# Kernel tuning notes

Hardware: AMD Instinct MI355X
Metric: run time of the kernel (lower is better)

The kernel has to match this reference:

```python
import jax, jax.numpy as jnp
import numpy as np

B, C, D, H, W = 1, 192, 32, 32, 32
NUM_HEADS = 6
KSZ = 3
DILATIONS = (1, 2, 3)
ND = len(DILATIONS)
HPD = NUM_HEADS // ND          # heads per dilation
HEAD_DIM = C // NUM_HEADS      # 32
CPD = C // ND                  # channels per dilation = HPD * HEAD_DIM
SCALE = HEAD_DIM ** -0.5
HIDDEN = int(C * 4.0)


def setup_inputs() -> dict:
    key = jax.random.key(0)
    ks = jax.random.split(key, 12)
    s = 0.02
    return {
        "x": jax.random.normal(ks[0], (B, C, H, W, D), jnp.float32),
        "qkv_w": jax.random.normal(ks[1], (3 * C, C), jnp.float32) * s,
        "proj_w": jax.random.normal(ks[2], (C, C), jnp.float32) * s,
        "proj_b": jnp.zeros((C,), jnp.float32),
        "g1": jnp.ones((C,), jnp.float32),
        "be1": jnp.zeros((C,), jnp.float32),
        "g2": jnp.ones((C,), jnp.float32),
        "be2": jnp.zeros((C,), jnp.float32),
        "w1": jax.random.normal(ks[3], (C, HIDDEN), jnp.float32) * s,
        "b1": jnp.zeros((HIDDEN,), jnp.float32),
        "w2": jax.random.normal(ks[4], (HIDDEN, C), jnp.float32) * s,
        "b2": jnp.zeros((C,), jnp.float32),
    }


def _layernorm(x, g, b, eps=1e-5):
    mu = jnp.mean(x, -1, keepdims=True)
    var = jnp.mean(jnp.square(x - mu), -1, keepdims=True)
    return (x - mu) * jax.lax.rsqrt(var + eps) * g + b


def _unfold3d(x, k, r):
    # x: [B, c, D, H, W] -> [k^3, B, c, D, H, W] of dilated local neighborhoods
    p = r * (k - 1) // 2
    xp = jnp.pad(x, ((0, 0), (0, 0), (p, p), (p, p), (p, p)))
    d, h, w = x.shape[2:]
    sl = [xp[:, :, i:i + d, j:j + h, l:l + w]
          for i in range(0, k * r, r)
          for j in range(0, k * r, r)
          for l in range(0, k * r, r)]
    return jnp.stack(sl, 0)


def _attn(x, qkv_w, proj_w, proj_b):
    # x: [B, D, H, W, C]
    x_cf = jnp.transpose(x, (0, 4, 1, 2, 3))                   # [B,C,D,H,W]
    qkv = jnp.einsum('oc,bczyx->bozyx', qkv_w, x_cf)
    qkv = qkv.reshape(B, 3, ND, CPD, D, H, W)
    outs = []
    for i, r in enumerate(DILATIONS):
        q = qkv[:, 0, i].reshape(B, HPD, HEAD_DIM, D, H, W)
        ku = _unfold3d(qkv[:, 1, i], KSZ, r).reshape(KSZ ** 3, B, HPD, HEAD_DIM, D, H, W)
        vu = _unfold3d(qkv[:, 2, i], KSZ, r).reshape(KSZ ** 3, B, HPD, HEAD_DIM, D, H, W)
        a = jnp.einsum('bnezyx,kbnezyx->bnzyxk', q, ku) * SCALE  # [B,n,D,H,W,27]
        a = jax.nn.softmax(a, axis=-1)
        o = jnp.einsum('bnzyxk,kbnezyx->bzyxne', a, vu).reshape(B, D, H, W, CPD)
        outs.append(o)
    out = jnp.concatenate(outs, -1)                            # [B,D,H,W,C] dilation-major
    return out @ proj_w + proj_b


def reference(x, qkv_w, proj_w, proj_b, g1, be1, g2, be2, w1, b1, w2, b2):
    # x: [B, C, H, W, D] -> [B, D, H, W, C]
    h = jnp.transpose(x, (0, 4, 2, 3, 1))
    h = h + _attn(_layernorm(h, g1, be1), qkv_w, proj_w, proj_b)
    m = _layernorm(h, g2, be2)
    m = jax.nn.gelu(m @ w1 + b1, approximate=False) @ w2 + b2
    h = h + m
    return jnp.transpose(h, (0, 4, 2, 3, 1))
```

## Files before the change

### kernel.cpp

```cpp
#include <hip/hip_runtime.h>
#include <hip/hip_bf16.h>
#include <math.h>

#define NV     32768
#define HIDDEN 768
#define SCALE  0.17677669529663687f

typedef __attribute__((ext_vector_type(8))) short short8;
typedef __attribute__((ext_vector_type(4))) float floatx4;
typedef __hip_bfloat16 bf16;

__device__ __forceinline__ void gload16(const void* g, void* l) {
    __builtin_amdgcn_global_load_lds(
        (const __attribute__((address_space(1))) unsigned int*)g,
        (__attribute__((address_space(3))) unsigned int*)l, 16, 0, 0);
}

__device__ __forceinline__ float bf2f(short s) {
    unsigned u = ((unsigned)(unsigned short)s) << 16;
    return __builtin_bit_cast(float, u);
}
__device__ __forceinline__ short f2bfs(float f) {
    bf16 b = __float2bfloat16(f);
    return *reinterpret_cast<short*>(&b);
}

__global__ __launch_bounds__(256) void prep_kernel(
        const float* __restrict__ qkv_w, const float* __restrict__ proj_w,
        const float* __restrict__ w1, const float* __restrict__ w2,
        bf16* __restrict__ wqkv, bf16* __restrict__ wproj,
        bf16* __restrict__ w1t, bf16* __restrict__ w2t) {
    int i = blockIdx.x * 256 + threadIdx.x;
    if (i < 110592) {
        wqkv[i] = (bf16)qkv_w[i];
    } else if (i < 147456) {
        int j = i - 110592; int r = j / 192, c = j - r * 192;
        wproj[c * 192 + r] = (bf16)proj_w[j];
    } else if (i < 294912) {
        int j = i - 147456; int r = j / 768, c = j - r * 768;
        w1t[c * 192 + r] = (bf16)w1[j];
    } else if (i < 442368) {
        int j = i - 294912; int r = j / 192, c = j - r * 192;
        w2t[c * 768 + r] = (bf16)w2[j];
    }
}

__global__ __launch_bounds__(256) void tin_ln_kernel(
        const float* __restrict__ xin, const float* __restrict__ g,
        const float* __restrict__ be, bf16* __restrict__ h,
        bf16* __restrict__ lnb) {
    __shared__ float lds[32 * 193];
    int yx = blockIdx.x;
    int y = yx >> 5, x = yx & 31;
    for (int idx = threadIdx.x; idx < 192 * 32; idx += 256) {
        int c = idx >> 5, z = idx & 31;
        lds[z * 193 + c] = xin[(((size_t)c * 32 + y) * 32 + x) * 32 + z];
    }
    __syncthreads();
    int wave = threadIdx.x >> 6, lane = threadIdx.x & 63;
    float ga = g[lane], gb = g[lane + 64], gc = g[lane + 128];
    float ba = be[lane], bb = be[lane + 64], bc = be[lane + 128];
    for (int z = wave; z < 32; z += 4) {
        float x0 = lds[z * 193 + lane];
        float x1 = lds[z * 193 + lane + 64];
        float x2 = lds[z * 193 + lane + 128];
        float s = x0 + x1 + x2;
        #pragma unroll
        for (int m = 32; m; m >>= 1) s += __shfl_xor(s, m);
        float mu = s * (1.f / 192.f);
        float d0 = x0 - mu, d1 = x1 - mu, d2 = x2 - mu;
        float s2 = d0 * d0 + d1 * d1 + d2 * d2;
        #pragma unroll
        for (int m = 32; m; m >>= 1) s2 += __shfl_xor(s2, m);
        float rstd = rsqrtf(s2 * (1.f / 192.f) + 1e-5f);
        size_t v = (size_t)((z << 10) + (y << 5) + x) * 192;
        h[v + lane]         = (bf16)x0;
        h[v + lane + 64]    = (bf16)x1;
        h[v + lane + 128]   = (bf16)x2;
        lnb[v + lane]       = (bf16)(d0 * rstd * ga + ba);
        lnb[v + lane + 64]  = (bf16)(d1 * rstd * gb + bb);
        lnb[v + lane + 128] = (bf16)(d2 * rstd * gc + bc);
    }
}

__global__ __launch_bounds__(256) void tout_kernel(const bf16* __restrict__ h,
                                                   float* __restrict__ outp) {
    __shared__ float lds[32 * 193];
    int yx = blockIdx.x;
    int y = yx >> 5, x = yx & 31;
    for (int idx = threadIdx.x; idx < 32 * 192; idx += 256) {
        int z = idx / 192, c = idx - z * 192;
        lds[z * 193 + c] = __bfloat162float(h[((size_t)((z * 32 + y) * 32 + x)) * 192 + c]);
    }
    __syncthreads();
    for (int idx = threadIdx.x; idx < 192 * 32; idx += 256) {
        int c = idx >> 5, z = idx & 31;
        outp[(((size_t)c * 32 + y) * 32 + x) * 32 + z] = lds[z * 193 + c];
    }
}

template <int MODE>
__global__ __launch_bounds__(256, 2) void mgemm_kernel(
        const bf16* __restrict__ A,
        const bf16* __restrict__ Bw,
        void* __restrict__ Cp,
        const float* __restrict__ bias,
        const bf16* __restrict__ res,
        int M, int N, int K) {
    __shared__ short Asm[128 * 64];
    __shared__ short Bsm[64 * 64];
    const int tid = threadIdx.x;
    const int lane = tid & 63;
    const int wave = tid >> 6;
    const int wm = wave >> 1, wn = wave & 1;
    const int m0 = blockIdx.x * 128;
    const int n0 = blockIdx.y * 64;

    const int srow = lane >> 3;
    const int scol = ((lane & 7) ^ ((lane >> 3) & 7)) * 16;

    floatx4 acc[4][2] = {};

    for (int k0 = 0; k0 < K; k0 += 64) {
        #pragma unroll
        for (int s = 0; s < 4; ++s) {
            int seg = wave * 4 + s;
            const char* g = (const char*)(A + (size_t)(m0 + seg * 8 + srow) * K + k0) + scol;
            gload16(g, (char*)Asm + seg * 1024);
        }
        #pragma unroll
        for (int s = 0; s < 2; ++s) {
            int seg = wave * 2 + s;
            const char* g = (const char*)(Bw + (size_t)(n0 + seg * 8 + srow) * K + k0) + scol;
            gload16(g, (char*)Bsm + seg * 1024);
        }
        __syncthreads();
        #pragma unroll
        for (int ks = 0; ks < 2; ++ks) {
            short8 af[4], bfr[2];
            const int cb = ks * 64 + (lane >> 4) * 16;
            #pragma unroll
            for (int i = 0; i < 4; ++i) {
                int row = wm * 64 + i * 16 + (lane & 15);
                af[i] = *reinterpret_cast<const short8*>(
                    (const char*)Asm + row * 128 + (cb ^ ((row & 7) << 4)));
            }
            #pragma unroll
            for (int j = 0; j < 2; ++j) {
                int row = wn * 32 + j * 16 + (lane & 15);
                bfr[j] = *reinterpret_cast<const short8*>(
                    (const char*)Bsm + row * 128 + (cb ^ ((row & 7) << 4)));
            }
            #pragma unroll
            for (int i = 0; i < 4; ++i)
                #pragma unroll
                for (int j = 0; j < 2; ++j)
                    acc[i][j] = __builtin_amdgcn_mfma_f32_16x16x32_bf16(
                        af[i], bfr[j], acc[i][j], 0, 0, 0);
        }
        __syncthreads();
    }

    const int r4 = (lane >> 4) * 4;
    const int cc = lane & 15;
    #pragma unroll
    for (int i = 0; i < 4; ++i) {
        #pragma unroll
        for (int j = 0; j < 2; ++j) {
            int colg = n0 + wn * 32 + j * 16 + cc;
            float bv = (MODE == 1 || MODE == 2) ? bias[colg] : 0.f;
            #pragma unroll
            for (int rg = 0; rg < 4; ++rg) {
                int rowg = m0 + wm * 64 + i * 16 + r4 + rg;
                float v = acc[i][j][rg];
                if (MODE == 1 || MODE == 2) v += bv;
                if (MODE == 2) v = 0.5f * v * (1.f + erff(v * 0.70710678118654752f));
                if (MODE == 1) {
                    v += __bfloat162float(res[(size_t)rowg * N + colg]);
                    ((bf16*)Cp)[(size_t)rowg * N + colg] = (bf16)v;
                } else if (MODE == 2) {
                    ((bf16*)Cp)[(size_t)rowg * N + colg] = (bf16)v;
                } else {
                    int part = colg / 192;
                    int rem  = colg - part * 192;
                    int di   = rem >> 6, hc = rem & 63;
                    size_t addr = (size_t)part * (6 * (size_t)NV * 32)
                                + (size_t)((di << 1) + (hc >> 5)) * ((size_t)NV * 32)
                                + (size_t)rowg * 32 + (hc & 31);
                    ((bf16*)Cp)[addr] = (bf16)v;
                }
            }
        }
    }
}

__global__ __launch_bounds__(256) void projln_kernel(
        const bf16* __restrict__ A, const bf16* __restrict__ Bw,
        bf16* __restrict__ hres, bf16* __restrict__ lnout,
        const float* __restrict__ bias,
        const float* __restrict__ g2, const float* __restrict__ be2) {
    __shared__ short Asm[64 * 64];
    __shared__ short Bsm[192 * 64];
    const int tid = threadIdx.x;
    const int lane = tid & 63;
    const int wave = tid >> 6;
    const int m0 = blockIdx.x * 64;

    const int srow = lane >> 3;
    const int scol = ((lane & 7) ^ ((lane >> 3) & 7)) * 16;

    floatx4 acc[12] = {};

    for (int k0 = 0; k0 < 192; k0 += 64) {
        #pragma unroll
        for (int s = 0; s < 2; ++s) {
            int seg = wave * 2 + s;
            const char* g = (const char*)(A + (size_t)(m0 + seg * 8 + srow) * 192 + k0) + scol;
            gload16(g, (char*)Asm + seg * 1024);
        }
        #pragma unroll
        for (int s = 0; s < 6; ++s) {
            int seg = wave * 6 + s;
            const char* g = (const char*)(Bw + (size_t)(seg * 8 + srow) * 192 + k0) + scol;
            gload16(g, (char*)Bsm + seg * 1024);
        }
        __syncthreads();
        #pragma unroll
        for (int ks = 0; ks < 2; ++ks) {
            const int cb = ks * 64 + (lane >> 4) * 16;
            int arow = wave * 16 + (lane & 15);
            short8 af = *reinterpret_cast<const short8*>(
                (const char*)Asm + arow * 128 + (cb ^ ((arow & 7) << 4)));
            #pragma unroll
            for (int j = 0; j < 12; ++j) {
                int brow = j * 16 + (lane & 15);
                short8 bfr = *reinterpret_cast<const short8*>(
                    (const char*)Bsm + brow * 128 + (cb ^ ((brow & 7) << 4)));
                acc[j] = __builtin_amdgcn_mfma_f32_16x16x32_bf16(af, bfr, acc[j], 0, 0, 0);
            }
        }
        __syncthreads();
    }

    const int cc = lane & 15;
    #pragma unroll
    for (int rg = 0; rg < 4; ++rg) {
        int rowg = m0 + wave * 16 + (lane >> 4) * 4 + rg;
        float vals[12];
        float vsum = 0.f;
        #pragma unroll
        for (int j = 0; j < 12; ++j) {
            int col = j * 16 + cc;
            float v = acc[j][rg] + bias[col]
                    + __bfloat162float(hres[(size_t)rowg * 192 + col]);
            vals[j] = v;
            vsum += v;
        }
        #pragma unroll
        for (int m = 8; m; m >>= 1) vsum += __shfl_xor(vsum, m);
        float mu = vsum * (1.f / 192.f);
        float vsq = 0.f;
        #pragma unroll
        for (int j = 0; j < 12; ++j) {
            float d = vals[j] - mu;
            vsq += d * d;
        }
        #pragma unroll
        for (int m = 8; m; m >>= 1) vsq += __shfl_xor(vsq, m);
        float rstd = rsqrtf(vsq * (1.f / 192.f) + 1e-5f);
        #pragma unroll
        for (int j = 0; j < 12; ++j) {
            int col = j * 16 + cc;
            hres[(size_t)rowg * 192 + col] = (bf16)vals[j];
            lnout[(size_t)rowg * 192 + col] =
                (bf16)((vals[j] - mu) * rstd * g2[col] + be2[col]);
        }
    }
}

__global__ __launch_bounds__(256) void attn_kernel(
        const bf16* __restrict__ qa,
        const bf16* __restrict__ ka,
        const bf16* __restrict__ va,
        bf16* __restrict__ attn_out) {
    const int lin = blockIdx.x;
    const int swz = (lin & 7) * 384 + (lin >> 3);
    const int dh  = swz >> 9;
    const int rp  = swz & 511;
    const int di = dh >> 1;
    const int r  = di + 1;
    const int wave = threadIdx.x >> 6, lane = threadIdx.x & 63;
    const int yz = rp * 2 + (wave >> 1);
    const int z = yz >> 5, y = yz & 31;
    const int x = ((wave & 1) << 4) + (lane >> 2);
    const int co = (lane & 3) << 3;
    const int v = (z << 10) + (y << 5) + x;

    const bf16* qb = qa + (size_t)dh * NV * 32 + co;
    const bf16* kb = ka + (size_t)dh * NV * 32 + co;
    const bf16* vb = va + (size_t)dh * NV * 32 + co;

    float qf[8];
    {
        short8 qv = *reinterpret_cast<const short8*>(qb + (size_t)v * 32);
        #pragma unroll
        for (int u = 0; u < 8; ++u) qf[u] = bf2f(qv[u]);
    }

    float o[8];
    #pragma unroll
    for (int c = 0; c < 8; ++c) o[c] = 0.f;
    float denom = 0.f;
    const float cexp = SCALE * 1.44269504088896f;

    #pragma unroll
    for (int kk = 0; kk < 27; ++kk) {
        const int dz = kk / 9 - 1, dy = (kk / 3) % 3 - 1, dx = kk % 3 - 1;
        int nz = z + dz * r, ny = y + dy * r, nx = x + dx * r;
        bool ok = ((unsigned)nz < 32u) & ((unsigned)ny < 32u) & ((unsigned)nx < 32u);
        int nv = ok ? v + r * ((dz << 10) + (dy << 5) + dx) : v;
        short8 kv = *reinterpret_cast<const short8*>(kb + (size_t)nv * 32);
        short8 vv = *reinterpret_cast<const short8*>(vb + (size_t)nv * 32);
        float d = 0.f;
        #pragma unroll
        for (int u = 0; u < 8; ++u) d += qf[u] * bf2f(kv[u]);
        d += __shfl_xor(d, 1);
        d += __shfl_xor(d, 2);
        float p = exp2f(ok ? d * cexp : 0.f);
        denom += p;
        float w = ok ? p : 0.f;
        #pragma unroll
        for (int u = 0; u < 8; ++u) o[u] += w * bf2f(vv[u]);
    }
    float inv = 1.f / denom;

    bf16* op = attn_out + (size_t)v * 192 + di * 64 + (dh & 1) * 32 + co;
    short8 st;
    #pragma unroll
    for (int u = 0; u < 8; ++u) st[u] = f2bfs(o[u] * inv);
    *reinterpret_cast<short8*>(op) = st;
}

extern "C" void kernel_launch(void* const* d_in, const int* in_sizes, int n_in,
                              void* d_out, int out_size, void* d_ws, size_t ws_size,
                              hipStream_t stream) {
    const float* x      = (const float*)d_in[0];
    const float* qkv_w  = (const float*)d_in[1];
    const float* proj_w = (const float*)d_in[2];
    const float* proj_b = (const float*)d_in[3];
    const float* g1     = (const float*)d_in[4];
    const float* be1    = (const float*)d_in[5];
    const float* g2     = (const float*)d_in[6];
    const float* be2    = (const float*)d_in[7];
    const float* w1     = (const float*)d_in[8];
    const float* b1     = (const float*)d_in[9];
    const float* w2     = (const float*)d_in[10];
    const float* b2     = (const float*)d_in[11];
    float* out = (float*)d_out;

    char* p = (char*)d_ws;
    bf16* h     = (bf16*)p;  p += (size_t)NV * 192 * 2;
    bf16* lnb   = (bf16*)p;  p += (size_t)NV * 192 * 2;
    bf16* qkvb  = (bf16*)p;  p += (size_t)NV * 576 * 2;
    bf16* attnb = (bf16*)p;  p += (size_t)NV * 192 * 2;
    bf16* tb    = qkvb;
    bf16* wqkv  = (bf16*)p;  p += (size_t)576 * 192 * 2;
    bf16* wproj = (bf16*)p;  p += (size_t)192 * 192 * 2;
    bf16* w1t   = (bf16*)p;  p += (size_t)768 * 192 * 2;
    bf16* w2t   = (bf16*)p;  p += (size_t)192 * 768 * 2;

    bf16* qa = qkvb;
    bf16* ka = qkvb + (size_t)6 * NV * 32;
    bf16* va = qkvb + (size_t)12 * NV * 32;

    prep_kernel<<<(442368 + 255) / 256, 256, 0, stream>>>(
        qkv_w, proj_w, w1, w2, wqkv, wproj, w1t, w2t);
    tin_ln_kernel<<<1024, 256, 0, stream>>>(x, g1, be1, h, lnb);

    mgemm_kernel<3><<<dim3(NV / 128, 576 / 64), 256, 0, stream>>>(
        lnb, wqkv, qkvb, nullptr, nullptr, NV, 576, 192);
    attn_kernel<<<3072, 256, 0, stream>>>(qa, ka, va, attnb);
    projln_kernel<<<NV / 64, 256, 0, stream>>>(
        attnb, wproj, h, lnb, proj_b, g2, be2);

    mgemm_kernel<2><<<dim3(NV / 128, HIDDEN / 64), 256, 0, stream>>>(
        lnb, w1t, tb, b1, nullptr, NV, HIDDEN, 192);
    mgemm_kernel<1><<<dim3(NV / 128, 192 / 64), 256, 0, stream>>>(
        tb, w2t, h, b2, h, NV, 192, HIDDEN);

    tout_kernel<<<1024, 256, 0, stream>>>(h, out);
}
```

Before: 149.8 us.

## Stage K/V neighbor rows in LDS and compute attention in packed fp16

The attention kernel now runs one block per (head, z, y) row. It loads the 9 neighboring K and V x-rows into shared memory with direct global-to-LDS loads, then reads neighbors from LDS instead of issuing scattered global loads. Q/K/V are stored as fp16 instead of bf16 so the dot products and the value accumulation can use packed half2 arithmetic. The risks are lower accumulation precision (fp16 output accumulators, fp16 weights) and the extra LDS traffic and barrier.

```diff
diff --git a/kernel.cpp b/kernel.cpp
--- a/kernel.cpp
+++ b/kernel.cpp
@@ -8,6 +8,8 @@
 
 typedef __attribute__((ext_vector_type(8))) short short8;
 typedef __attribute__((ext_vector_type(4))) float floatx4;
+typedef __attribute__((ext_vector_type(8))) _Float16 h8;
+typedef __attribute__((ext_vector_type(2))) _Float16 h2;
 typedef __hip_bfloat16 bf16;
 
 __device__ __forceinline__ void gload16(const void* g, void* l) {
@@ -187,7 +189,7 @@
                     size_t addr = (size_t)part * (6 * (size_t)NV * 32)
                                 + (size_t)((di << 1) + (hc >> 5)) * ((size_t)NV * 32)
                                 + (size_t)rowg * 32 + (hc & 31);
-                    ((bf16*)Cp)[addr] = (bf16)v;
+                    ((_Float16*)Cp)[addr] = (_Float16)v;
                 }
             }
         }
@@ -278,66 +280,84 @@
     }
 }
 
-__global__ __launch_bounds__(256) void attn_kernel(
-        const bf16* __restrict__ qa,
-        const bf16* __restrict__ ka,
-        const bf16* __restrict__ va,
+__global__ __launch_bounds__(128) void attn_kernel(
+        const _Float16* __restrict__ qa,
+        const _Float16* __restrict__ ka,
+        const _Float16* __restrict__ va,
         bf16* __restrict__ attn_out) {
+    __shared__ _Float16 lds[18432];
     const int lin = blockIdx.x;
-    const int swz = (lin & 7) * 384 + (lin >> 3);
-    const int dh  = swz >> 9;
-    const int rp  = swz & 511;
+    const int swz = (lin & 7) * 768 + (lin >> 3);
+    const int dh  = swz >> 10;
+    const int yz  = swz & 1023;
     const int di = dh >> 1;
     const int r  = di + 1;
-    const int wave = threadIdx.x >> 6, lane = threadIdx.x & 63;
-    const int yz = rp * 2 + (wave >> 1);
     const int z = yz >> 5, y = yz & 31;
-    const int x = ((wave & 1) << 4) + (lane >> 2);
-    const int co = (lane & 3) << 3;
+    const int t = threadIdx.x;
+
+    const _Float16* kb = ka + (size_t)dh * NV * 32;
+    const _Float16* vb = va + (size_t)dh * NV * 32;
+
+    #pragma unroll
+    for (int s = 0; s < 18; ++s) {
+        const int sr = s % 9;
+        const int dz = sr / 3 - 1, dy = sr % 3 - 1;
+        int zz = z + dz * r, yy = y + dy * r;
+        zz = zz < 0 ? 0 : (zz > 31 ? 31 : zz);
+        yy = yy < 0 ? 0 : (yy > 31 ? 31 : yy);
+        const _Float16* src = (s < 9 ? kb : vb)
+                            + (size_t)(((zz << 10) + (yy << 5)) * 32);
+        gload16((const char*)src + t * 16,
+                (char*)lds + s * 2048 + (t >> 6) * 1024);
+    }
+
+    const int x = t >> 2, c4 = t & 3;
     const int v = (z << 10) + (y << 5) + x;
-
-    const bf16* qb = qa + (size_t)dh * NV * 32 + co;
-    const bf16* kb = ka + (size_t)dh * NV * 32 + co;
-    const bf16* vb = va + (size_t)dh * NV * 32 + co;
-
-    float qf[8];
-    {
-        short8 qv = *reinterpret_cast<const short8*>(qb + (size_t)v * 32);
-        #pragma unroll
-        for (int u = 0; u < 8; ++u) qf[u] = bf2f(qv[u]);
-    }
-
-    float o[8];
-    #pragma unroll
-    for (int c = 0; c < 8; ++c) o[c] = 0.f;
+    h8 q8 = *reinterpret_cast<const h8*>(qa + ((size_t)dh * NV + v) * 32 + c4 * 8);
+    h2 q01 = {q8[0], q8[1]}, q23 = {q8[2], q8[3]};
+    h2 q45 = {q8[4], q8[5]}, q67 = {q8[6], q8[7]};
+
+    __syncthreads();
+
     float denom = 0.f;
+    h2 o01 = {0, 0}, o23 = {0, 0}, o45 = {0, 0}, o67 = {0, 0};
     const float cexp = SCALE * 1.44269504088896f;
 
     #pragma unroll
     for (int kk = 0; kk < 27; ++kk) {
         const int dz = kk / 9 - 1, dy = (kk / 3) % 3 - 1, dx = kk % 3 - 1;
+        const int slot = (dz + 1) * 3 + (dy + 1);
         int nz = z + dz * r, ny = y + dy * r, nx = x + dx * r;
         bool ok = ((unsigned)nz < 32u) & ((unsigned)ny < 32u) & ((unsigned)nx < 32u);
-        int nv = ok ? v + r * ((dz << 10) + (dy << 5) + dx) : v;
-        short8 kv = *reinterpret_cast<const short8*>(kb + (size_t)nv * 32);
-        short8 vv = *reinterpret_cast<const short8*>(vb + (size_t)nv * 32);
-        float d = 0.f;
-        #pragma unroll
-        for (int u = 0; u < 8; ++u) d += qf[u] * bf2f(kv[u]);
+        int rx = ok ? nx : x;
+        const char* kaddr = (const char*)lds + slot * 2048 + rx * 64 + c4 * 16;
+        h8 k8 = *reinterpret_cast<const h8*>(kaddr);
+        h8 v8 = *reinterpret_cast<const h8*>(kaddr + 9 * 2048);
+        h2 a = q01 * (h2){k8[0], k8[1]};
+        a = q23 * (h2){k8[2], k8[3]} + a;
+        a = q45 * (h2){k8[4], k8[5]} + a;
+        a = q67 * (h2){k8[6], k8[7]} + a;
+        float d = (float)a[0] + (float)a[1];
         d += __shfl_xor(d, 1);
         d += __shfl_xor(d, 2);
         float p = exp2f(ok ? d * cexp : 0.f);
         denom += p;
         float w = ok ? p : 0.f;
-        #pragma unroll
-        for (int u = 0; u < 8; ++u) o[u] += w * bf2f(vv[u]);
+        _Float16 wh = (_Float16)w;
+        h2 w2 = {wh, wh};
+        o01 = w2 * (h2){v8[0], v8[1]} + o01;
+        o23 = w2 * (h2){v8[2], v8[3]} + o23;
+        o45 = w2 * (h2){v8[4], v8[5]} + o45;
+        o67 = w2 * (h2){v8[6], v8[7]} + o67;
     }
     float inv = 1.f / denom;
 
-    bf16* op = attn_out + (size_t)v * 192 + di * 64 + (dh & 1) * 32 + co;
+    bf16* op = attn_out + (size_t)v * 192 + di * 64 + (dh & 1) * 32 + c4 * 8;
     short8 st;
-    #pragma unroll
-    for (int u = 0; u < 8; ++u) st[u] = f2bfs(o[u] * inv);
+    st[0] = f2bfs((float)o01[0] * inv); st[1] = f2bfs((float)o01[1] * inv);
+    st[2] = f2bfs((float)o23[0] * inv); st[3] = f2bfs((float)o23[1] * inv);
+    st[4] = f2bfs((float)o45[0] * inv); st[5] = f2bfs((float)o45[1] * inv);
+    st[6] = f2bfs((float)o67[0] * inv); st[7] = f2bfs((float)o67[1] * inv);
     *reinterpret_cast<short8*>(op) = st;
 }
 
@@ -369,9 +389,9 @@
     bf16* w1t   = (bf16*)p;  p += (size_t)768 * 192 * 2;
     bf16* w2t   = (bf16*)p;  p += (size_t)192 * 768 * 2;
 
-    bf16* qa = qkvb;
-    bf16* ka = qkvb + (size_t)6 * NV * 32;
-    bf16* va = qkvb + (size_t)12 * NV * 32;
+    _Float16* qa = (_Float16*)qkvb;
+    _Float16* ka = qa + (size_t)6 * NV * 32;
+    _Float16* va = qa + (size_t)12 * NV * 32;
 
     prep_kernel<<<(442368 + 255) / 256, 256, 0, stream>>>(
         qkv_w, proj_w, w1, w2, wqkv, wproj, w1t, w2t);
@@ -379,7 +399,7 @@
 
     mgemm_kernel<3><<<dim3(NV / 128, 576 / 64), 256, 0, stream>>>(
         lnb, wqkv, qkvb, nullptr, nullptr, NV, 576, 192);
-    attn_kernel<<<3072, 256, 0, stream>>>(qa, ka, va, attnb);
+    attn_kernel<<<6144, 128, 0, stream>>>(qa, ka, va, attnb);
     projln_kernel<<<NV / 64, 256, 0, stream>>>(
         attnb, wproj, h, lnb, proj_b, g2, be2);
 
```

After: 135.1 us. -9.8%, faster.
